# Optimization experiments

Hardware: AMD Instinct MI355X
Metric: run time of the kernel (lower is better)

The kernel has to match this reference:

```python
import jax, jax.numpy as jnp
import numpy as np

I, H, O = 4096, 4096, 50257


def gru_cell(x, h, w_ih, w_hh, b_ih, b_hh):
    # x: [1, in], h: [1, H]; PyTorch GRU gate order: r, z, n
    gi = x @ w_ih.T + b_ih          # [1, 3H]
    gh = h @ w_hh.T + b_hh          # [1, 3H]
    i_r, i_z, i_n = jnp.split(gi, 3, axis=1)
    h_r, h_z, h_n = jnp.split(gh, 3, axis=1)
    r = jax.nn.sigmoid(i_r + h_r)
    z = jax.nn.sigmoid(i_z + h_z)
    n = jnp.tanh(i_n + r * h_n)
    return (1.0 - z) * n + z * h    # [1, H]


def setup_inputs() -> dict:
    key = jax.random.key(0)
    ks = jax.random.split(key, 12)
    s = 1.0 / np.sqrt(H)
    u = lambda k, shape: jax.random.uniform(k, shape, jnp.float32, -s, s)
    return {
        "input": jax.random.normal(ks[0], (1, 1, I), jnp.float32),
        "hidden": jax.random.normal(ks[1], (1, 1, H), jnp.float32),
        "w_ih1": u(ks[2], (3 * H, I)),
        "w_hh1": u(ks[3], (3 * H, H)),
        "b_ih1": u(ks[4], (3 * H,)),
        "b_hh1": u(ks[5], (3 * H,)),
        "w_ih2": u(ks[6], (3 * H, H)),
        "w_hh2": u(ks[7], (3 * H, H)),
        "b_ih2": u(ks[8], (3 * H,)),
        "b_hh2": u(ks[9], (3 * H,)),
        "w_out": u(ks[10], (O, H)),
        "b_out": u(ks[11], (O,)),
    }


def reference(input, hidden, w_ih1, w_hh1, b_ih1, b_hh1,
              w_ih2, w_hh2, b_ih2, b_hh2, w_out, b_out):
    x = input.reshape(1, I)         # seq=1, batch=1 -> [1, I]
    h0 = hidden.reshape(1, H)
    # GRU layer 1 (single step)
    h1 = gru_cell(x, h0, w_ih1, w_hh1, b_ih1, b_hh1)
    # GRU layer 2: the original feeds GRU1's output AND its hidden (identical
    # tensors for a 1-step, 1-layer GRU) into the second GRU.
    h2 = gru_cell(h1, h1, w_ih2, w_hh2, b_ih2, b_hh2)
    out = jax.nn.relu(h2)            # output[:, 0] -> [1, H]
    out = out @ w_out.T + b_out      # [1, O]
    out = jax.nn.log_softmax(out, axis=1)
    return out, h2.reshape(1, 1, H)
```

## Files before the change

### kernel.cpp

```cpp
#include <hip/hip_runtime.h>
#include <math.h>

#define HDIM 4096
#define ODIM 50257
#define G3H  12288
#define NBLK 2048
#define NTHR 256

typedef float f32x4 __attribute__((ext_vector_type(4)));


__device__ __forceinline__ float wave_reduce_sum(float v) {
#pragma unroll
    for (int off = 32; off > 0; off >>= 1) v += __shfl_down(v, off, 64);
    return v;
}

__device__ __forceinline__ float dot_row(const float* __restrict__ Wrow,
                                         const f32x4* __restrict__ vs,
                                         int lane) {
    const f32x4* w4 = reinterpret_cast<const f32x4*>(Wrow);
    float acc0 = 0.f, acc1 = 0.f;
#pragma unroll
    for (int t = 0; t < 16; t += 2) {
        f32x4 a0 = __builtin_nontemporal_load(&w4[t * 64 + lane]);
        f32x4 b0 = vs[t * 64 + lane];
        f32x4 a1 = __builtin_nontemporal_load(&w4[(t + 1) * 64 + lane]);
        f32x4 b1 = vs[(t + 1) * 64 + lane];
        acc0 = fmaf(a0.x, b0.x, acc0);
        acc0 = fmaf(a0.y, b0.y, acc0);
        acc0 = fmaf(a0.z, b0.z, acc0);
        acc0 = fmaf(a0.w, b0.w, acc0);
        acc1 = fmaf(a1.x, b1.x, acc1);
        acc1 = fmaf(a1.y, b1.y, acc1);
        acc1 = fmaf(a1.z, b1.z, acc1);
        acc1 = fmaf(a1.w, b1.w, acc1);
    }
    return wave_reduce_sum(acc0 + acc1);
}


__global__ __launch_bounds__(NTHR) void gemv_dual(
    const float* __restrict__ Wa, const float* __restrict__ va,
    const float* __restrict__ ba, float* __restrict__ oa,
    const float* __restrict__ Wb, const float* __restrict__ vb,
    const float* __restrict__ bb, float* __restrict__ ob) {
    __shared__ f32x4 vs[HDIM / 4];
    const bool isB = blockIdx.x >= (NBLK / 2);
    const float* W  = isB ? Wb : Wa;
    const float* v  = isB ? vb : va;
    const float* bs = isB ? bb : ba;
    float*       o  = isB ? ob : oa;
    const int blk = isB ? (int)blockIdx.x - NBLK / 2 : (int)blockIdx.x;

    const f32x4* v4 = reinterpret_cast<const f32x4*>(v);
#pragma unroll
    for (int i = 0; i < 4; ++i)
        vs[i * NTHR + threadIdx.x] = v4[i * NTHR + threadIdx.x];
    __syncthreads();

    const int wid = threadIdx.x >> 6, lane = threadIdx.x & 63;
    const int row0 = blk * 12 + wid * 3;
#pragma unroll
    for (int r = 0; r < 3; ++r) {
        int row = row0 + r;
        float d = dot_row(&W[(size_t)row * HDIM], vs, lane);
        if (lane == 0) o[row] = d + bs[row];
    }
}

__global__ void gru_gate(const float* __restrict__ gi, const float* __restrict__ gh,
                         const float* __restrict__ hprev, float* __restrict__ hout,
                         float* __restrict__ act) {
    int j = blockIdx.x * blockDim.x + threadIdx.x;
    if (j < HDIM) {
        float r = 1.f / (1.f + expf(-(gi[j] + gh[j])));
        float z = 1.f / (1.f + expf(-(gi[HDIM + j] + gh[HDIM + j])));
        float n = tanhf(gi[2 * HDIM + j] + r * gh[2 * HDIM + j]);
        float h = (1.f - z) * n + z * hprev[j];
        hout[j] = h;
        if (act) act[j] = fmaxf(h, 0.f);
    }
}

__global__ __launch_bounds__(NTHR) void gemv_logits_lse(
    const float* __restrict__ W, const float* __restrict__ v,
    const float* __restrict__ bias, float* __restrict__ out,
    float2* __restrict__ pairs) {
    __shared__ f32x4 vs[HDIM / 4];
    __shared__ float smx[4], ssm[4];

    const f32x4* v4 = reinterpret_cast<const f32x4*>(v);
#pragma unroll
    for (int i = 0; i < 4; ++i)
        vs[i * NTHR + threadIdx.x] = v4[i * NTHR + threadIdx.x];
    __syncthreads();

    const int b = blockIdx.x;
    const int start = b * 24 + min(b, 1105);
    const int cnt   = 24 + (b < 1105 ? 1 : 0);
    const int wid = threadIdx.x >> 6, lane = threadIdx.x & 63;
    const int wq = cnt >> 2, wr = cnt & 3;
    const int woff = wid * wq + min(wid, wr);
    const int wcnt = wq + (wid < wr ? 1 : 0);

    float m = -INFINITY, s = 0.f;
    for (int r = 0; r < wcnt; ++r) {
        int row = start + woff + r;
        float d = dot_row(&W[(size_t)row * HDIM], vs, lane);
        if (lane == 0) {
            float val = d + bias[row];
            out[row] = val;
            if (val > m) { s = s * expf(m - val) + 1.f; m = val; }
            else         { s += expf(val - m); }
        }
    }
    if (lane == 0) { smx[wid] = m; ssm[wid] = s; }
    __syncthreads();
    if (threadIdx.x == 0) {
        float M = smx[0], S = ssm[0];
#pragma unroll
        for (int i = 1; i < 4; ++i) {
            float mi = smx[i], si = ssm[i];
            if (mi > M) { S = S * expf(M - mi) + si; M = mi; }
            else        { S += si * expf(mi - M); }
        }
        pairs[b] = make_float2(M, S);
    }
}

__global__ __launch_bounds__(NTHR) void logsm_final(
    float* __restrict__ out, const float2* __restrict__ pairs) {
    __shared__ float smx[4], ssm[4];
    __shared__ float lc;
    float m = -INFINITY, s = 0.f;
    for (int i = threadIdx.x; i < NBLK; i += NTHR) {
        float2 p = pairs[i];
        if (p.x > m) { s = s * expf(m - p.x) + p.y; m = p.x; }
        else         { s += p.y * expf(p.x - m); }
    }
#pragma unroll
    for (int off = 32; off > 0; off >>= 1) {
        float mo = __shfl_down(m, off, 64);
        float so = __shfl_down(s, off, 64);
        if (mo > m) { s = s * expf(m - mo) + so; m = mo; }
        else        { s += so * expf(mo - m); }
    }
    const int wid = threadIdx.x >> 6, lane = threadIdx.x & 63;
    if (lane == 0) { smx[wid] = m; ssm[wid] = s; }
    __syncthreads();
    if (threadIdx.x == 0) {
        float M = smx[0], S = ssm[0];
#pragma unroll
        for (int i = 1; i < 4; ++i) {
            float mi = smx[i], si = ssm[i];
            if (mi > M) { S = S * expf(M - mi) + si; M = mi; }
            else        { S += si * expf(mi - M); }
        }
        lc = M + logf(S);
    }
    __syncthreads();
    float logC = lc;
    for (int i = blockIdx.x * NTHR + threadIdx.x; i < ODIM; i += gridDim.x * NTHR)
        out[i] -= logC;
}


extern "C" void kernel_launch(void* const* d_in, const int* in_sizes, int n_in,
                              void* d_out, int out_size, void* d_ws, size_t ws_size,
                              hipStream_t stream) {
    const float* x     = (const float*)d_in[0];
    const float* h0    = (const float*)d_in[1];
    const float* w_ih1 = (const float*)d_in[2];
    const float* w_hh1 = (const float*)d_in[3];
    const float* b_ih1 = (const float*)d_in[4];
    const float* b_hh1 = (const float*)d_in[5];
    const float* w_ih2 = (const float*)d_in[6];
    const float* w_hh2 = (const float*)d_in[7];
    const float* b_ih2 = (const float*)d_in[8];
    const float* b_hh2 = (const float*)d_in[9];
    const float* w_out = (const float*)d_in[10];
    const float* b_out = (const float*)d_in[11];

    float* out    = (float*)d_out;
    float* h2_out = out + ODIM;

    float* ws   = (float*)d_ws;
    float* gi1  = ws;
    float* gh1  = ws + 12288;
    float* gi2  = ws + 24576;
    float* gh2  = ws + 36864;
    float* h1   = ws + 49152;
    float* act  = ws + 53248;
    float2* pairs = (float2*)(ws + 57344);

    gemv_dual<<<NBLK, NTHR, 0, stream>>>(w_ih1, x, b_ih1, gi1,
                                         w_hh1, h0, b_hh1, gh1);
    gru_gate<<<HDIM / NTHR, NTHR, 0, stream>>>(gi1, gh1, h0, h1, nullptr);

    gemv_dual<<<NBLK, NTHR, 0, stream>>>(w_ih2, h1, b_ih2, gi2,
                                         w_hh2, h1, b_hh2, gh2);
    gru_gate<<<HDIM / NTHR, NTHR, 0, stream>>>(gi2, gh2, h1, h2_out, act);

    gemv_logits_lse<<<NBLK, NTHR, 0, stream>>>(w_out, act, b_out, out, pairs);
    logsm_final<<<64, NTHR, 0, stream>>>(out, pairs);
}
```

Measured before the change: 265.9 us.

## Fuse GRU pipeline into one persistent cooperative kernel with grid syncs

Replaces the six separate launches with a single cooperative kernel of 512 blocks that runs both GRU layers, gates, logits GEMV and log-softmax normalization, separated by grid.sync. Each block now processes many more rows per stage. The intent is to remove launch gaps and inter-kernel drain/fill, at the cost of lower occupancy, grid-wide barriers, and idle blocks during the gate stages. It keeps the old multi-kernel path as a fallback if the cooperative launch fails.

New measurement: 585.2 us. 2.2x slower.

```diff
diff --git a/kernel.cpp b/kernel.cpp
--- a/kernel.cpp
+++ b/kernel.cpp
@@ -1,20 +1,17 @@
 #include <hip/hip_runtime.h>
+#include <hip/hip_cooperative_groups.h>
 #include <math.h>
+
+namespace cg = cooperative_groups;
 
 #define HDIM 4096
 #define ODIM 50257
-#define G3H  12288
-#define NBLK 2048
 #define NTHR 256
+#define CBLK 512
+#define FBLK 2048
 
 typedef float f32x4 __attribute__((ext_vector_type(4)));
 
-
-__device__ __forceinline__ float wave_reduce_sum(float v) {
-#pragma unroll
-    for (int off = 32; off > 0; off >>= 1) v += __shfl_down(v, off, 64);
-    return v;
-}
 
 __device__ __forceinline__ float dot_row(const float* __restrict__ Wrow,
                                          const f32x4* __restrict__ vs,
@@ -36,7 +33,165 @@
         acc1 = fmaf(a1.z, b1.z, acc1);
         acc1 = fmaf(a1.w, b1.w, acc1);
     }
-    return wave_reduce_sum(acc0 + acc1);
+    float v = acc0 + acc1;
+#pragma unroll
+    for (int off = 32; off > 0; off >>= 1) v += __shfl_down(v, off, 64);
+    return v;
+}
+
+__device__ __forceinline__ void stage_v(f32x4* vs, const float* __restrict__ v) {
+    const f32x4* v4 = reinterpret_cast<const f32x4*>(v);
+#pragma unroll
+    for (int i = 0; i < 4; ++i)
+        vs[i * NTHR + threadIdx.x] = v4[i * NTHR + threadIdx.x];
+}
+
+__device__ __forceinline__ float gate_one(const float* __restrict__ gi,
+                                          const float* __restrict__ gh,
+                                          float hprev, int j) {
+    float r = 1.f / (1.f + expf(-(gi[j] + gh[j])));
+    float z = 1.f / (1.f + expf(-(gi[HDIM + j] + gh[HDIM + j])));
+    float n = tanhf(gi[2 * HDIM + j] + r * gh[2 * HDIM + j]);
+    return (1.f - z) * n + z * hprev;
+}
+
+__device__ __forceinline__ void lse_absorb(float& m, float& s, float mo, float so) {
+    if (mo > m) { s = s * expf(m - mo) + so; m = mo; }
+    else        { s += so * expf(mo - m); }
+}
+
+
+__global__ __launch_bounds__(NTHR, 2) void mega(
+    const float* __restrict__ x, const float* __restrict__ h0,
+    const float* __restrict__ w_ih1, const float* __restrict__ w_hh1,
+    const float* __restrict__ b_ih1, const float* __restrict__ b_hh1,
+    const float* __restrict__ w_ih2, const float* __restrict__ w_hh2,
+    const float* __restrict__ b_ih2, const float* __restrict__ b_hh2,
+    const float* __restrict__ w_out, const float* __restrict__ b_out,
+    float* __restrict__ out, float* __restrict__ ws) {
+    cg::grid_group grid = cg::this_grid();
+    __shared__ f32x4 vs[HDIM / 4];
+    __shared__ float smx[4], ssm[4], lds_lc;
+
+    float* gi1 = ws;
+    float* gh1 = ws + 12288;
+    float* gi2 = ws + 24576;
+    float* gh2 = ws + 36864;
+    float* h1  = ws + 49152;
+    float* act = ws + 53248;
+    float2* pairs = (float2*)(ws + 57344);
+    float* h2g = out + ODIM;
+
+    const int bid = blockIdx.x, tid = threadIdx.x;
+    const int wid = tid >> 6, lane = tid & 63;
+
+    {
+        const bool hi = bid >= (CBLK / 2);
+        const float* W  = hi ? w_hh1 : w_ih1;
+        const float* vv = hi ? h0 : x;
+        const float* bb = hi ? b_hh1 : b_ih1;
+        float* o = hi ? gh1 : gi1;
+        const int blk = bid & (CBLK / 2 - 1);
+        stage_v(vs, vv);
+        __syncthreads();
+        const int row0 = blk * 48 + wid * 12;
+#pragma unroll
+        for (int r = 0; r < 12; ++r) {
+            int row = row0 + r;
+            float d = dot_row(&W[(size_t)row * HDIM], vs, lane);
+            if (lane == 0) o[row] = d + bb[row];
+        }
+    }
+    grid.sync();
+
+    if (bid < 16) {
+        int j = bid * NTHR + tid;
+        h1[j] = gate_one(gi1, gh1, h0[j], j);
+    }
+    grid.sync();
+
+    {
+        const bool hi = bid >= (CBLK / 2);
+        const float* W  = hi ? w_hh2 : w_ih2;
+        const float* bb = hi ? b_hh2 : b_ih2;
+        float* o = hi ? gh2 : gi2;
+        const int blk = bid & (CBLK / 2 - 1);
+        stage_v(vs, h1);
+        __syncthreads();
+        const int row0 = blk * 48 + wid * 12;
+#pragma unroll
+        for (int r = 0; r < 12; ++r) {
+            int row = row0 + r;
+            float d = dot_row(&W[(size_t)row * HDIM], vs, lane);
+            if (lane == 0) o[row] = d + bb[row];
+        }
+    }
+    grid.sync();
+
+    if (bid < 16) {
+        int j = bid * NTHR + tid;
+        float h2 = gate_one(gi2, gh2, h1[j], j);
+        h2g[j] = h2;
+        act[j] = fmaxf(h2, 0.f);
+    }
+    grid.sync();
+
+    {
+        stage_v(vs, act);
+        __syncthreads();
+        const int start = bid * 98 + min(bid, 81);
+        const int cnt   = 98 + (bid < 81 ? 1 : 0);
+        const int wq = cnt >> 2, wr = cnt & 3;
+        const int woff = wid * wq + min(wid, wr);
+        const int wcnt = wq + (wid < wr ? 1 : 0);
+        float m = -INFINITY, s = 0.f;
+        for (int r = 0; r < wcnt; ++r) {
+            int row = start + woff + r;
+            float d = dot_row(&w_out[(size_t)row * HDIM], vs, lane);
+            if (lane == 0) {
+                float val = d + b_out[row];
+                out[row] = val;
+                if (val > m) { s = s * expf(m - val) + 1.f; m = val; }
+                else         { s += expf(val - m); }
+            }
+        }
+        if (lane == 0) { smx[wid] = m; ssm[wid] = s; }
+        __syncthreads();
+        if (tid == 0) {
+            float M = smx[0], S = ssm[0];
+#pragma unroll
+            for (int i = 1; i < 4; ++i) lse_absorb(M, S, smx[i], ssm[i]);
+            pairs[bid] = make_float2(M, S);
+        }
+    }
+    grid.sync();
+
+    {
+        float m = -INFINITY, s = 0.f;
+#pragma unroll
+        for (int i = 0; i < CBLK / NTHR; ++i) {
+            float2 p = pairs[tid + i * NTHR];
+            lse_absorb(m, s, p.x, p.y);
+        }
+#pragma unroll
+        for (int off = 32; off > 0; off >>= 1) {
+            float mo = __shfl_down(m, off, 64);
+            float so = __shfl_down(s, off, 64);
+            lse_absorb(m, s, mo, so);
+        }
+        if (lane == 0) { smx[wid] = m; ssm[wid] = s; }
+        __syncthreads();
+        if (tid == 0) {
+            float M = smx[0], S = ssm[0];
+#pragma unroll
+            for (int i = 1; i < 4; ++i) lse_absorb(M, S, smx[i], ssm[i]);
+            lds_lc = M + logf(S);
+        }
+        __syncthreads();
+        const float logC = lds_lc;
+        int i = bid * NTHR + tid;
+        if (i < ODIM) out[i] -= logC;
+    }
 }
 
 
@@ -46,17 +201,14 @@
     const float* __restrict__ Wb, const float* __restrict__ vb,
     const float* __restrict__ bb, float* __restrict__ ob) {
     __shared__ f32x4 vs[HDIM / 4];
-    const bool isB = blockIdx.x >= (NBLK / 2);
+    const bool isB = blockIdx.x >= (FBLK / 2);
     const float* W  = isB ? Wb : Wa;
     const float* v  = isB ? vb : va;
     const float* bs = isB ? bb : ba;
     float*       o  = isB ? ob : oa;
-    const int blk = isB ? (int)blockIdx.x - NBLK / 2 : (int)blockIdx.x;
-
-    const f32x4* v4 = reinterpret_cast<const f32x4*>(v);
-#pragma unroll
-    for (int i = 0; i < 4; ++i)
-        vs[i * NTHR + threadIdx.x] = v4[i * NTHR + threadIdx.x];
+    const int blk = isB ? (int)blockIdx.x - FBLK / 2 : (int)blockIdx.x;
+
+    stage_v(vs, v);
     __syncthreads();
 
     const int wid = threadIdx.x >> 6, lane = threadIdx.x & 63;
@@ -74,10 +226,7 @@
                          float* __restrict__ act) {
     int j = blockIdx.x * blockDim.x + threadIdx.x;
     if (j < HDIM) {
-        float r = 1.f / (1.f + expf(-(gi[j] + gh[j])));
-        float z = 1.f / (1.f + expf(-(gi[HDIM + j] + gh[HDIM + j])));
-        float n = tanhf(gi[2 * HDIM + j] + r * gh[2 * HDIM + j]);
-        float h = (1.f - z) * n + z * hprev[j];
+        float h = gate_one(gi, gh, hprev[j], j);
         hout[j] = h;
         if (act) act[j] = fmaxf(h, 0.f);
     }
@@ -90,10 +239,7 @@
     __shared__ f32x4 vs[HDIM / 4];
     __shared__ float smx[4], ssm[4];
 
-    const f32x4* v4 = reinterpret_cast<const f32x4*>(v);
-#pragma unroll
-    for (int i = 0; i < 4; ++i)
-        vs[i * NTHR + threadIdx.x] = v4[i * NTHR + threadIdx.x];
+    stage_v(vs, v);
     __syncthreads();
 
     const int b = blockIdx.x;
@@ -120,11 +266,7 @@
     if (threadIdx.x == 0) {
         float M = smx[0], S = ssm[0];
 #pragma unroll
-        for (int i = 1; i < 4; ++i) {
-            float mi = smx[i], si = ssm[i];
-            if (mi > M) { S = S * expf(M - mi) + si; M = mi; }
-            else        { S += si * expf(mi - M); }
-        }
+        for (int i = 1; i < 4; ++i) lse_absorb(M, S, smx[i], ssm[i]);
         pairs[b] = make_float2(M, S);
     }
 }
@@ -134,17 +276,15 @@
     __shared__ float smx[4], ssm[4];
     __shared__ float lc;
     float m = -INFINITY, s = 0.f;
-    for (int i = threadIdx.x; i < NBLK; i += NTHR) {
+    for (int i = threadIdx.x; i < FBLK; i += NTHR) {
         float2 p = pairs[i];
-        if (p.x > m) { s = s * expf(m - p.x) + p.y; m = p.x; }
-        else         { s += p.y * expf(p.x - m); }
+        lse_absorb(m, s, p.x, p.y);
     }
 #pragma unroll
     for (int off = 32; off > 0; off >>= 1) {
         float mo = __shfl_down(m, off, 64);
         float so = __shfl_down(s, off, 64);
-        if (mo > m) { s = s * expf(m - mo) + so; m = mo; }
-        else        { s += so * expf(mo - m); }
+        lse_absorb(m, s, mo, so);
     }
     const int wid = threadIdx.x >> 6, lane = threadIdx.x & 63;
     if (lane == 0) { smx[wid] = m; ssm[wid] = s; }
@@ -152,11 +292,7 @@
     if (threadIdx.x == 0) {
         float M = smx[0], S = ssm[0];
 #pragma unroll
-        for (int i = 1; i < 4; ++i) {
-            float mi = smx[i], si = ssm[i];
-            if (mi > M) { S = S * expf(M - mi) + si; M = mi; }
-            else        { S += si * expf(mi - M); }
-        }
+        for (int i = 1; i < 4; ++i) lse_absorb(M, S, smx[i], ssm[i]);
         lc = M + logf(S);
     }
     __syncthreads();
@@ -181,11 +317,21 @@
     const float* b_hh2 = (const float*)d_in[9];
     const float* w_out = (const float*)d_in[10];
     const float* b_out = (const float*)d_in[11];
-
-    float* out    = (float*)d_out;
-    float* h2_out = out + ODIM;
-
-    float* ws   = (float*)d_ws;
+    float* out = (float*)d_out;
+    float* ws  = (float*)d_ws;
+
+    void* args[] = {
+        (void*)&x, (void*)&h0,
+        (void*)&w_ih1, (void*)&w_hh1, (void*)&b_ih1, (void*)&b_hh1,
+        (void*)&w_ih2, (void*)&w_hh2, (void*)&b_ih2, (void*)&b_hh2,
+        (void*)&w_out, (void*)&b_out,
+        (void*)&out, (void*)&ws
+    };
+    hipError_t err = hipLaunchCooperativeKernel((const void*)mega, dim3(CBLK),
+                                                dim3(NTHR), args, 0, stream);
+    if (err == hipSuccess) return;
+    (void)hipGetLastError();
+
     float* gi1  = ws;
     float* gh1  = ws + 12288;
     float* gi2  = ws + 24576;
@@ -193,15 +339,14 @@
     float* h1   = ws + 49152;
     float* act  = ws + 53248;
     float2* pairs = (float2*)(ws + 57344);
-
-    gemv_dual<<<NBLK, NTHR, 0, stream>>>(w_ih1, x, b_ih1, gi1,
+    float* h2_out = out + ODIM;
+
+    gemv_dual<<<FBLK, NTHR, 0, stream>>>(w_ih1, x, b_ih1, gi1,
                                          w_hh1, h0, b_hh1, gh1);
     gru_gate<<<HDIM / NTHR, NTHR, 0, stream>>>(gi1, gh1, h0, h1, nullptr);
-
-    gemv_dual<<<NBLK, NTHR, 0, stream>>>(w_ih2, h1, b_ih2, gi2,
+    gemv_dual<<<FBLK, NTHR, 0, stream>>>(w_ih2, h1, b_ih2, gi2,
                                          w_hh2, h1, b_hh2, gh2);
     gru_gate<<<HDIM / NTHR, NTHR, 0, stream>>>(gi2, gh2, h1, h2_out, act);
-
-    gemv_logits_lse<<<NBLK, NTHR, 0, stream>>>(w_out, act, b_out, out, pairs);
+    gemv_logits_lse<<<FBLK, NTHR, 0, stream>>>(w_out, act, b_out, out, pairs);
     logsm_final<<<64, NTHR, 0, stream>>>(out, pairs);
 }
```

## Fuse GRU gate into gemv kernel via per-unit arrival counters

Applied to the files above, without the earlier changes.

Rows are reassigned so each block computes the r, z and n gate rows for the same four hidden units. The ih/hh block pair signals completion through an atomic counter, and the last-arriving block applies the GRU gate math. This removes the two separate gate kernel launches and their inter-kernel gaps. In exchange it adds a memset for the flags, atomics, fences, and a strided row access pattern across the weight matrix.

Measured after the change: 1.020 ms. +283.4%, slower.

```diff
diff --git a/kernel.cpp b/kernel.cpp
--- a/kernel.cpp
+++ b/kernel.cpp
@@ -3,18 +3,13 @@
 
 #define HDIM 4096
 #define ODIM 50257
-#define G3H  12288
-#define NBLK 2048
 #define NTHR 256
+#define GBLK 2048
 
 typedef float f32x4 __attribute__((ext_vector_type(4)));
 
 
-__device__ __forceinline__ float wave_reduce_sum(float v) {
-#pragma unroll
-    for (int off = 32; off > 0; off >>= 1) v += __shfl_down(v, off, 64);
-    return v;
-}
+__device__ __forceinline__ float sigm(float v) { return 1.f / (1.f + expf(-v)); }
 
 __device__ __forceinline__ float dot_row(const float* __restrict__ Wrow,
                                          const f32x4* __restrict__ vs,
@@ -36,50 +31,71 @@
         acc1 = fmaf(a1.z, b1.z, acc1);
         acc1 = fmaf(a1.w, b1.w, acc1);
     }
-    return wave_reduce_sum(acc0 + acc1);
-}
-
-
-__global__ __launch_bounds__(NTHR) void gemv_dual(
-    const float* __restrict__ Wa, const float* __restrict__ va,
-    const float* __restrict__ ba, float* __restrict__ oa,
-    const float* __restrict__ Wb, const float* __restrict__ vb,
-    const float* __restrict__ bb, float* __restrict__ ob) {
-    __shared__ f32x4 vs[HDIM / 4];
-    const bool isB = blockIdx.x >= (NBLK / 2);
-    const float* W  = isB ? Wb : Wa;
-    const float* v  = isB ? vb : va;
-    const float* bs = isB ? bb : ba;
-    float*       o  = isB ? ob : oa;
-    const int blk = isB ? (int)blockIdx.x - NBLK / 2 : (int)blockIdx.x;
-
+    float v = acc0 + acc1;
+#pragma unroll
+    for (int off = 32; off > 0; off >>= 1) v += __shfl_down(v, off, 64);
+    return v;
+}
+
+__device__ __forceinline__ void stage_v(f32x4* vs, const float* __restrict__ v) {
     const f32x4* v4 = reinterpret_cast<const f32x4*>(v);
 #pragma unroll
     for (int i = 0; i < 4; ++i)
         vs[i * NTHR + threadIdx.x] = v4[i * NTHR + threadIdx.x];
-    __syncthreads();
-
-    const int wid = threadIdx.x >> 6, lane = threadIdx.x & 63;
-    const int row0 = blk * 12 + wid * 3;
+}
+
+__device__ __forceinline__ void lse_absorb(float& m, float& s, float mo, float so) {
+    if (mo > m) { s = s * expf(m - mo) + so; m = mo; }
+    else        { s += so * expf(mo - m); }
+}
+
+__device__ __forceinline__ float ldA(const float* p) {
+    return __hip_atomic_load(p, __ATOMIC_RELAXED, __HIP_MEMORY_SCOPE_AGENT);
+}
+__device__ __forceinline__ void stA(float* p, float v) {
+    __hip_atomic_store(p, v, __ATOMIC_RELAXED, __HIP_MEMORY_SCOPE_AGENT);
+}
+
+__global__ __launch_bounds__(NTHR) void gemv_gate(
+    const float* __restrict__ Wih, const float* __restrict__ vih,
+    const float* __restrict__ bih, float* __restrict__ gi,
+    const float* __restrict__ Whh, const float* __restrict__ vhh,
+    const float* __restrict__ bhh, float* __restrict__ gh,
+    const float* __restrict__ hprev, float* __restrict__ hout,
+    float* __restrict__ actout, int* __restrict__ flags) {
+    __shared__ f32x4 vs[HDIM / 4];
+    __shared__ int second;
+    const bool hiB = blockIdx.x >= (GBLK / 2);
+    stage_v(vs, hiB ? vhh : vih);
+    __syncthreads();
+
+    const float* W  = hiB ? Whh : Wih;
+    const float* bb = hiB ? bhh : bih;
+    float*       o  = hiB ? gh : gi;
+    const int b = (int)blockIdx.x & (GBLK / 2 - 1);
+    const int tid = threadIdx.x, wid = tid >> 6, lane = tid & 63;
+    const int j = b * 4 + wid;
+
 #pragma unroll
     for (int r = 0; r < 3; ++r) {
-        int row = row0 + r;
+        int row = j + r * HDIM;
         float d = dot_row(&W[(size_t)row * HDIM], vs, lane);
-        if (lane == 0) o[row] = d + bs[row];
-    }
-}
-
-__global__ void gru_gate(const float* __restrict__ gi, const float* __restrict__ gh,
-                         const float* __restrict__ hprev, float* __restrict__ hout,
-                         float* __restrict__ act) {
-    int j = blockIdx.x * blockDim.x + threadIdx.x;
-    if (j < HDIM) {
-        float r = 1.f / (1.f + expf(-(gi[j] + gh[j])));
-        float z = 1.f / (1.f + expf(-(gi[HDIM + j] + gh[HDIM + j])));
-        float n = tanhf(gi[2 * HDIM + j] + r * gh[2 * HDIM + j]);
-        float h = (1.f - z) * n + z * hprev[j];
+        if (lane == 0) stA(&o[row], d + bb[row]);
+    }
+    __threadfence();
+    __syncthreads();
+    if (tid == 0) second = (atomicAdd(&flags[b], 1) == 1);
+    __syncthreads();
+    if (second && lane == 0) {
+        float gir = ldA(&gi[j]),            ghr = ldA(&gh[j]);
+        float giz = ldA(&gi[j + HDIM]),     ghz = ldA(&gh[j + HDIM]);
+        float gin = ldA(&gi[j + 2 * HDIM]), ghn = ldA(&gh[j + 2 * HDIM]);
+        float rr = sigm(gir + ghr);
+        float zz = sigm(giz + ghz);
+        float nn = tanhf(gin + rr * ghn);
+        float h  = (1.f - zz) * nn + zz * hprev[j];
         hout[j] = h;
-        if (act) act[j] = fmaxf(h, 0.f);
+        if (actout) actout[j] = fmaxf(h, 0.f);
     }
 }
 
@@ -89,11 +105,7 @@
     float2* __restrict__ pairs) {
     __shared__ f32x4 vs[HDIM / 4];
     __shared__ float smx[4], ssm[4];
-
-    const f32x4* v4 = reinterpret_cast<const f32x4*>(v);
-#pragma unroll
-    for (int i = 0; i < 4; ++i)
-        vs[i * NTHR + threadIdx.x] = v4[i * NTHR + threadIdx.x];
+    stage_v(vs, v);
     __syncthreads();
 
     const int b = blockIdx.x;
@@ -120,11 +132,7 @@
     if (threadIdx.x == 0) {
         float M = smx[0], S = ssm[0];
 #pragma unroll
-        for (int i = 1; i < 4; ++i) {
-            float mi = smx[i], si = ssm[i];
-            if (mi > M) { S = S * expf(M - mi) + si; M = mi; }
-            else        { S += si * expf(mi - M); }
-        }
+        for (int i = 1; i < 4; ++i) lse_absorb(M, S, smx[i], ssm[i]);
         pairs[b] = make_float2(M, S);
     }
 }
@@ -134,17 +142,15 @@
     __shared__ float smx[4], ssm[4];
     __shared__ float lc;
     float m = -INFINITY, s = 0.f;
-    for (int i = threadIdx.x; i < NBLK; i += NTHR) {
+    for (int i = threadIdx.x; i < GBLK; i += NTHR) {
         float2 p = pairs[i];
-        if (p.x > m) { s = s * expf(m - p.x) + p.y; m = p.x; }
-        else         { s += p.y * expf(p.x - m); }
+        lse_absorb(m, s, p.x, p.y);
     }
 #pragma unroll
     for (int off = 32; off > 0; off >>= 1) {
         float mo = __shfl_down(m, off, 64);
         float so = __shfl_down(s, off, 64);
-        if (mo > m) { s = s * expf(m - mo) + so; m = mo; }
-        else        { s += so * expf(mo - m); }
+        lse_absorb(m, s, mo, so);
     }
     const int wid = threadIdx.x >> 6, lane = threadIdx.x & 63;
     if (lane == 0) { smx[wid] = m; ssm[wid] = s; }
@@ -152,11 +158,7 @@
     if (threadIdx.x == 0) {
         float M = smx[0], S = ssm[0];
 #pragma unroll
-        for (int i = 1; i < 4; ++i) {
-            float mi = smx[i], si = ssm[i];
-            if (mi > M) { S = S * expf(M - mi) + si; M = mi; }
-            else        { S += si * expf(mi - M); }
-        }
+        for (int i = 1; i < 4; ++i) lse_absorb(M, S, smx[i], ssm[i]);
         lc = M + logf(S);
     }
     __syncthreads();
@@ -190,18 +192,20 @@
     float* gh1  = ws + 12288;
     float* gi2  = ws + 24576;
     float* gh2  = ws + 36864;
-    float* h1   = ws + 49152;
+    float* h1g  = ws + 49152;
     float* act  = ws + 53248;
     float2* pairs = (float2*)(ws + 57344);
-
-    gemv_dual<<<NBLK, NTHR, 0, stream>>>(w_ih1, x, b_ih1, gi1,
-                                         w_hh1, h0, b_hh1, gh1);
-    gru_gate<<<HDIM / NTHR, NTHR, 0, stream>>>(gi1, gh1, h0, h1, nullptr);
-
-    gemv_dual<<<NBLK, NTHR, 0, stream>>>(w_ih2, h1, b_ih2, gi2,
-                                         w_hh2, h1, b_hh2, gh2);
-    gru_gate<<<HDIM / NTHR, NTHR, 0, stream>>>(gi2, gh2, h1, h2_out, act);
-
-    gemv_logits_lse<<<NBLK, NTHR, 0, stream>>>(w_out, act, b_out, out, pairs);
+    int* flag1  = (int*)(ws + 61440);
+    int* flag2  = (int*)(ws + 62464);
+
+    hipMemsetAsync(flag1, 0, 2048 * sizeof(int), stream);
+
+    gemv_gate<<<GBLK, NTHR, 0, stream>>>(w_ih1, x, b_ih1, gi1,
+                                         w_hh1, h0, b_hh1, gh1,
+                                         h0, h1g, nullptr, flag1);
+    gemv_gate<<<GBLK, NTHR, 0, stream>>>(w_ih2, h1g, b_ih2, gi2,
+                                         w_hh2, h1g, b_hh2, gh2,
+                                         h1g, h2_out, act, flag2);
+    gemv_logits_lse<<<GBLK, NTHR, 0, stream>>>(w_out, act, b_out, out, pairs);
     logsm_final<<<64, NTHR, 0, stream>>>(out, pairs);
 }
```
